# Performance work log

Measured on AMD Instinct MI355X. Metric: run time of the kernel, lower is better.

The kernel has to match this reference:

```python
import jax, jax.numpy as jnp
import numpy as np

D = 1024      # dim_input
H = 16        # n_heads
DH = 64       # dim_inner
S = 1024      # current_seq
M = 1024      # pre_seq (memory)
B = 2         # batch
SCALE = 1.0 / np.sqrt(DH)


def _rel_shift(x):
    # x: [S, J, B, H]; Transformer-XL relative shift
    s, j = x.shape[0], x.shape[1]
    zero = jnp.zeros((s, 1) + x.shape[2:], x.dtype)
    x = jnp.concatenate([zero, x], axis=1)            # [S, J+1, B, H]
    x = x.reshape((j + 1, s) + x.shape[2:])[1:]        # [J, S, B, H]
    return x.reshape((s, j) + x.shape[2:])             # [S, J, B, H]


def setup_inputs() -> dict:
    key = jax.random.key(0)
    ks = jax.random.split(key, 9)
    std = 1.0 / np.sqrt(D)
    return {
        "multi_head_input": jax.random.normal(ks[0], (S, B, D), jnp.float32),
        "position_emb": jax.random.normal(ks[1], (S + M, D), jnp.float32),
        "memory": jax.random.normal(ks[2], (M, B, D), jnp.float32),
        "u": jax.random.normal(ks[3], (H, DH), jnp.float32) * 0.02,
        "v": jax.random.normal(ks[4], (H, DH), jnp.float32) * 0.02,
        "W_kv": jax.random.normal(ks[5], (D, 2 * H * DH), jnp.float32) * std,
        "W_q": jax.random.normal(ks[6], (D, H * DH), jnp.float32) * std,
        "W_pos": jax.random.normal(ks[7], (D, H * DH), jnp.float32) * std,
        "W_out": jax.random.normal(ks[8], (H * DH, D), jnp.float32) * std,
    }


def reference(multi_head_input, position_emb, memory, u, v, W_kv, W_q, W_pos, W_out):
    s = multi_head_input.shape[0]
    m = memory.shape[0]
    b = multi_head_input.shape[1]
    x_mem = jnp.concatenate([memory, multi_head_input], axis=0)   # [M+S, B, D]
    kv = x_mem @ W_kv                                              # [M+S, B, 2*H*DH]
    k, val = jnp.split(kv, 2, axis=-1)
    k = k.reshape(m + s, b, H, DH)
    val = val.reshape(m + s, b, H, DH)
    q = (multi_head_input @ W_q).reshape(s, b, H, DH)              # [S, B, H, DH]

    # content term: (q + u) . k
    content = jnp.einsum('ibhd,jbhd->ijbh', q + u, k)              # [S, M+S, B, H]
    # position term: (q + v) . r, then rel_shift
    r = (position_emb @ W_pos).reshape(m + s, H, DH)               # [M+S, H, DH]
    pos = jnp.einsum('ibhd,jhd->ijbh', q + v, r)                   # [S, M+S, B, H]
    pos = _rel_shift(pos)

    attn = jax.nn.softmax((content + pos) * SCALE, axis=1)         # [S, M+S, B, H]
    out = jnp.einsum('ijbh,jbhd->ibhd', attn, val).reshape(s, b, H * DH)
    return out @ W_out                                             # [S, B, D]
```

## Files before the change

### kernel.cpp

```cpp
#include <hip/hip_runtime.h>
#include <hip/hip_bf16.h>
#include <hip/hip_fp16.h>
#include <math.h>

#define D    1024
#define H    16
#define DH   64
#define S    1024
#define M    1024
#define B    2
#define J    2048
#define SCALE 0.125f

typedef __attribute__((ext_vector_type(8))) short        bf16x8;
typedef __attribute__((ext_vector_type(4))) short        s16x4;
typedef __attribute__((ext_vector_type(8))) _Float16     h16x8;
typedef __attribute__((ext_vector_type(8))) unsigned short us8;
typedef __attribute__((ext_vector_type(4))) float        f32x4;

__device__ __forceinline__ short f2bs(float f) {
    __hip_bfloat16 t = __float2bfloat16(f);
    short r; __builtin_memcpy(&r, &t, 2); return r;
}
__device__ __forceinline__ unsigned short f2bf_fast(float f) {
    unsigned int u; __builtin_memcpy(&u, &f, 4);
    return (unsigned short)((u + 0x8000u) >> 16);
}

__device__ __forceinline__ void g2l16(const short* g, short* l) {
    __builtin_amdgcn_global_load_lds(
        (const __attribute__((address_space(1))) unsigned int*)g,
        (__attribute__((address_space(3))) unsigned int*)l, 16, 0, 0);
}

__global__ __launch_bounds__(256)
void prep(const float* __restrict__ mem, const float* __restrict__ x,
          const float* __restrict__ pemb,
          const float* __restrict__ Wkv, const float* __restrict__ Wq,
          const float* __restrict__ Wpos, const float* __restrict__ Wout,
          short* __restrict__ a_bf, short* __restrict__ p_bf,
          short* __restrict__ wkvt, short* __restrict__ wqt,
          short* __restrict__ wpt,  short* __restrict__ wot)
{
    __shared__ float t[64][65];
    int blk = blockIdx.x;
    const int tid = threadIdx.x;
    if (blk < 6144) {
        const int idx = (blk * 256 + tid) * 4;
        const int TWO_M = 2 * 1024 * 1024;
        float4 v; short* dst;
        if (idx < TWO_M)          { v = *(const float4*)(mem  + idx);           dst = a_bf + idx; }
        else if (idx < 2 * TWO_M) { v = *(const float4*)(x    + idx - TWO_M);   dst = a_bf + idx; }
        else                      { v = *(const float4*)(pemb + idx - 2*TWO_M); dst = p_bf + idx - 2*TWO_M; }
        s16x4 o = { f2bs(v.x), f2bs(v.y), f2bs(v.z), f2bs(v.w) };
        *(s16x4*)dst = o;
        return;
    }
    blk -= 6144;
    const float* src; short* dst; int N, t0;
    if (blk < 512)       { src = Wkv;  dst = wkvt; N = 2048; t0 = blk; }
    else if (blk < 768)  { src = Wq;   dst = wqt;  N = 1024; t0 = blk - 512; }
    else if (blk < 1024) { src = Wpos; dst = wpt;  N = 1024; t0 = blk - 768; }
    else                 { src = Wout; dst = wot;  N = 1024; t0 = blk - 1024; }
    const int ntn = N >> 6;
    const int k0 = (t0 / ntn) * 64, n0 = (t0 % ntn) * 64;
    #pragma unroll
    for (int e = tid; e < 4096; e += 256) {
        int r = e >> 6, c = e & 63;
        t[r][c] = src[(size_t)(k0 + r) * N + n0 + c];
    }
    __syncthreads();
    #pragma unroll
    for (int e = tid; e < 4096; e += 256) {
        int nr = e >> 6, kc = e & 63;
        dst[(size_t)(n0 + nr) * 1024 + k0 + kc] = f2bs(t[kc][nr]);
    }
}

__device__ __forceinline__ void gemm_core(const short* __restrict__ A,
                                          const short* __restrict__ Bt,
                                          short* As, short* Bs,
                                          int bm0, int bn0, int tid,
                                          f32x4 acc[4][4])
{
    const int w    = tid >> 6;
    const int wy   = w >> 1, wx = w & 1;
    const int lane = tid & 63;
    const int lm   = lane & 15;
    const int lq   = lane >> 4;

    for (int k0 = 0; k0 < 1024; k0 += 64) {
        const short* Ab = A  + (size_t)bm0 * 1024 + k0;
        const short* Bb = Bt + (size_t)bn0 * 1024 + k0;
        #pragma unroll
        for (int t = 0; t < 4; ++t) {
            int s = t * 256 + tid;
            int r = s >> 3, c = s & 7;
            int cg = c ^ (r & 7);
            g2l16(Ab + r * 1024 + cg * 8, As + s * 8);
            g2l16(Bb + r * 1024 + cg * 8, Bs + s * 8);
        }
        __syncthreads();
        #pragma unroll
        for (int kk = 0; kk < 2; ++kk) {
            bf16x8 af[4], bg[4];
            #pragma unroll
            for (int r4 = 0; r4 < 4; ++r4) {
                int ar = wy * 64 + r4 * 16 + lm;
                int kc = kk * 4 + lq;
                af[r4] = *(const bf16x8*)(As + ((ar << 3) + (kc ^ (ar & 7))) * 8);
            }
            #pragma unroll
            for (int c4 = 0; c4 < 4; ++c4) {
                int br = wx * 64 + c4 * 16 + lm;
                int kc = kk * 4 + lq;
                bg[c4] = *(const bf16x8*)(Bs + ((br << 3) + (kc ^ (br & 7))) * 8);
            }
            #pragma unroll
            for (int r4 = 0; r4 < 4; ++r4)
                #pragma unroll
                for (int c4 = 0; c4 < 4; ++c4)
                    acc[r4][c4] = __builtin_amdgcn_mfma_f32_16x16x32_bf16(
                        af[r4], bg[c4], acc[r4][c4], 0, 0, 0);
        }
        __syncthreads();
    }
}

__global__ __launch_bounds__(256)
void proj_fused(const short* __restrict__ a_bf, const short* __restrict__ p_bf,
                const short* __restrict__ wkvt, const short* __restrict__ wqt,
                const short* __restrict__ wpt,
                short* __restrict__ k_bf, short* __restrict__ vt_bf,
                short* __restrict__ qu_bf, short* __restrict__ qv_bf,
                short* __restrict__ r_bf,
                const float* __restrict__ uvec, const float* __restrict__ vvec)
{
    __shared__ __align__(16) short As[128 * 64];
    __shared__ __align__(16) short Bs[128 * 64];

    int blk = blockIdx.x;
    int mode, bx, by;
    const short *A, *Bt;
    if (blk < 512)      { bx = blk & 15; by = blk >> 4;
                          if (bx >= 8) { mode = 4; A = wkvt; Bt = a_bf; }
                          else         { mode = 0; A = a_bf; Bt = wkvt; } }
    else if (blk < 640) { int b2 = blk - 512; mode = 1; bx = b2 & 7; by = b2 >> 3;
                          A = a_bf + (size_t)2048 * 1024; Bt = wqt; }
    else                { int b3 = blk - 640; mode = 2; bx = b3 & 7; by = b3 >> 3;
                          A = p_bf; Bt = wpt; }
    const int bn0 = (mode == 4) ? by * 128 : bx * 128;
    const int bm0 = (mode == 4) ? bx * 128 : by * 128;
    const int tid = threadIdx.x;
    const int w = tid >> 6, wy = w >> 1, wx = w & 1;
    const int lane = tid & 63, lm = lane & 15, lq = lane >> 4;

    f32x4 acc[4][4];
    #pragma unroll
    for (int r = 0; r < 4; ++r)
        #pragma unroll
        for (int c = 0; c < 4; ++c) acc[r][c] = (f32x4){0.f, 0.f, 0.f, 0.f};

    gemm_core(A, Bt, As, Bs, bm0, bn0, tid, acc);

    #pragma unroll
    for (int r4 = 0; r4 < 4; ++r4) {
        #pragma unroll
        for (int c4 = 0; c4 < 4; ++c4) {
            const int n = bn0 + wx * 64 + c4 * 16 + lm;
            float ubias = 0.f, vbias = 0.f;
            if (mode == 1) { ubias = uvec[n]; vbias = vvec[n]; }
            #pragma unroll
            for (int reg = 0; reg < 4; ++reg) {
                const int m = bm0 + wy * 64 + r4 * 16 + lq * 4 + reg;
                const float val = acc[r4][c4][reg];
                if (mode == 0) {
                    int j = m >> 1, b = m & 1;
                    int h = n >> 6, d = n & 63;
                    k_bf[(((size_t)b * H + h) * J + j) * DH + d] = f2bs(val);
                } else if (mode == 4) {
                    int n2 = m - 1024, h = n2 >> 6, d = n2 & 63;
                    int j = n >> 1, b = n & 1;
                    vt_bf[(((size_t)b * H + h) * DH + d) * J + j] = f2bs(val);
                } else if (mode == 1) {
                    int i = m >> 1, b = m & 1;
                    int h = n >> 6, d = n & 63;
                    size_t o = (((size_t)b * H + h) * S + i) * DH + d;
                    qu_bf[o] = f2bs((val + ubias) * SCALE);
                    qv_bf[o] = f2bs((val + vbias) * SCALE);
                } else {
                    int h = n >> 6, d = n & 63;
                    r_bf[((size_t)h * J + m) * DH + d] = f2bs(val);
                }
            }
        }
    }
}

__global__ __launch_bounds__(256)
void gemm_out(const short* __restrict__ A, const short* __restrict__ Bt,
              float* __restrict__ out)
{
    __shared__ __align__(16) short As[128 * 64];
    __shared__ __align__(16) short Bs[128 * 64];
    const int bn0 = blockIdx.x * 128, bm0 = blockIdx.y * 128;
    const int tid = threadIdx.x;
    const int w = tid >> 6, wy = w >> 1, wx = w & 1;
    const int lane = tid & 63, lm = lane & 15, lq = lane >> 4;

    f32x4 acc[4][4];
    #pragma unroll
    for (int r = 0; r < 4; ++r)
        #pragma unroll
        for (int c = 0; c < 4; ++c) acc[r][c] = (f32x4){0.f, 0.f, 0.f, 0.f};

    gemm_core(A, Bt, As, Bs, bm0, bn0, tid, acc);

    #pragma unroll
    for (int r4 = 0; r4 < 4; ++r4)
        #pragma unroll
        for (int c4 = 0; c4 < 4; ++c4) {
            const int n = bn0 + wx * 64 + c4 * 16 + lm;
            #pragma unroll
            for (int reg = 0; reg < 4; ++reg) {
                const int m = bm0 + wy * 64 + r4 * 16 + lq * 4 + reg;
                out[(size_t)m * 1024 + n] = acc[r4][c4][reg];
            }
        }
}

__device__ __forceinline__ int sidx(int m, int c) {
    return (m << 10) + (c ^ (m << 3));
}

__global__ __launch_bounds__(512)
void attn_mfma(const short* __restrict__ qu_bf, const short* __restrict__ qv_bf,
               const short* __restrict__ k_bf,  const short* __restrict__ vt_bf,
               const short* __restrict__ r_bf,
               float* __restrict__ opart, float* __restrict__ lsum)
{
    __shared__ __align__(16) unsigned short sc[32 * 1024];
    __half* sch = (__half*)sc;
    float*  scF = (float*)sc;

    const int bh  = blockIdx.x;
    const int it  = blockIdx.y;
    const int jh  = blockIdx.z;
    const int i0  = it * 32;
    const int cbeg = jh << 10, cend = cbeg + 1024;
    const int h   = bh & (H - 1);
    const int tid = threadIdx.x;
    const int w    = tid >> 6;
    const int lane = tid & 63;
    const int lm   = lane & 15;
    const int lq   = lane >> 4;
    const int slot = (it * 32 + bh) * 2 + jh;

    const short* qup0 = qu_bf + ((size_t)(bh * S + i0 + lm)) * DH + lq * 8;
    const short* qup1 = qup0 + 16 * DH;
    bf16x8 au00 = *(const bf16x8*)qup0,        au01 = *(const bf16x8*)(qup0 + 32);
    bf16x8 au10 = *(const bf16x8*)qup1,        au11 = *(const bf16x8*)(qup1 + 32);
    const short* qvp0 = qv_bf + ((size_t)(bh * S + i0 + lm)) * DH + lq * 8;
    const short* qvp1 = qvp0 + 16 * DH;
    bf16x8 av00 = *(const bf16x8*)qvp0,        av01 = *(const bf16x8*)(qvp0 + 32);
    bf16x8 av10 = *(const bf16x8*)qvp1,        av11 = *(const bf16x8*)(qvp1 + 32);
    int r1a = i0 + 1 + lm;  if (r1a > S - 1) r1a = S - 1;
    int r1b = i0 + 17 + lm; if (r1b > S - 1) r1b = S - 1;
    const short* qwp0 = qv_bf + ((size_t)(bh * S + r1a)) * DH + lq * 8;
    const short* qwp1 = qv_bf + ((size_t)(bh * S + r1b)) * DH + lq * 8;
    bf16x8 aw00 = *(const bf16x8*)qwp0,        aw01 = *(const bf16x8*)(qwp0 + 32);
    bf16x8 aw10 = *(const bf16x8*)qwp1,        aw11 = *(const bf16x8*)(qwp1 + 32);

    if (tid < 32) {
        int hole = i0 + tid + 1025;
        if (hole >= cbeg && hole < cend) sc[sidx(tid, hole - cbeg)] = 0;
    }

    const short* rbase = r_bf + (size_t)h * J * DH;

    {
        int tmp = cbeg + 977 - i0;
        int tlo = tmp > 0 ? ((tmp + 15) >> 4) : 0;
        int thi = (cend + 1022 - i0) >> 4; if (thi > 127) thi = 127;
        for (int t = tlo + w; t <= thi; t += 8) {
            const short* rp = rbase + (size_t)(t * 16 + lm) * DH + lq * 8;
            bf16x8 b0 = *(const bf16x8*)rp, b1 = *(const bf16x8*)(rp + 32);
            f32x4 c0 = {0.f,0.f,0.f,0.f}, c1 = {0.f,0.f,0.f,0.f};
            c0 = __builtin_amdgcn_mfma_f32_16x16x32_bf16(av00, b0, c0, 0, 0, 0);
            c1 = __builtin_amdgcn_mfma_f32_16x16x32_bf16(av10, b0, c1, 0, 0, 0);
            c0 = __builtin_amdgcn_mfma_f32_16x16x32_bf16(av01, b1, c0, 0, 0, 0);
            c1 = __builtin_amdgcn_mfma_f32_16x16x32_bf16(av11, b1, c1, 0, 0, 0);
            int cb = i0 + t * 16 + lm - 1023 - cbeg;
            int base = i0 + 16 * t - 1023;
            if (base >= cbeg && base + 46 < cend) {
                #pragma unroll
                for (int r = 0; r < 4; ++r) {
                    int m0 = lq * 4 + r, m1 = m0 + 16;
                    sch[sidx(m0, cb + m0)] = __float2half(c0[r]);
                    sch[sidx(m1, cb + m1)] = __float2half(c1[r]);
                }
            } else {
                #pragma unroll
                for (int r = 0; r < 4; ++r) {
                    int m0 = lq * 4 + r, m1 = m0 + 16;
                    int cA = cb + m0, cB = cb + m1;
                    if (cA >= 0 && cA < 1024) sch[sidx(m0, cA)] = __float2half(c0[r]);
                    if (cB >= 0 && cB < 1024) sch[sidx(m1, cB)] = __float2half(c1[r]);
                }
            }
        }
    }

    {
        int tmpw = cbeg - 1072 - i0;
        int tlw = tmpw > 0 ? ((tmpw + 15) >> 4) : 0;
        int thw = (cend - 1027 - i0) >> 4; if (thw > 127) thw = 127;
        for (int t = tlw + w; t <= thw; t += 8) {
            const short* rp = rbase + (size_t)(t * 16 + lm) * DH + lq * 8;
            bf16x8 b0 = *(const bf16x8*)rp, b1 = *(const bf16x8*)(rp + 32);
            f32x4 c0 = {0.f,0.f,0.f,0.f}, c1 = {0.f,0.f,0.f,0.f};
            c0 = __builtin_amdgcn_mfma_f32_16x16x32_bf16(aw00, b0, c0, 0, 0, 0);
            c1 = __builtin_amdgcn_mfma_f32_16x16x32_bf16(aw10, b0, c1, 0, 0, 0);
            c0 = __builtin_amdgcn_mfma_f32_16x16x32_bf16(aw01, b1, c0, 0, 0, 0);
            c1 = __builtin_amdgcn_mfma_f32_16x16x32_bf16(aw11, b1, c1, 0, 0, 0);
            int cb = i0 + t * 16 + lm + 1026 - cbeg;
            int base = i0 + 16 * t + 1026;
            if (base >= cbeg && base + 46 < cend) {
                #pragma unroll
                for (int r = 0; r < 4; ++r) {
                    int m0 = lq * 4 + r, m1 = m0 + 16;
                    sch[sidx(m0, cb + m0)] = __float2half(c0[r]);
                    sch[sidx(m1, cb + m1)] = __float2half(c1[r]);
                }
            } else {
                #pragma unroll
                for (int r = 0; r < 4; ++r) {
                    int m0 = lq * 4 + r, m1 = m0 + 16;
                    int cA = cb + m0, cB = cb + m1;
                    if (cA >= 0 && cA < 1024) sch[sidx(m0, cA)] = __float2half(c0[r]);
                    if (cB >= 0 && cB < 1024) sch[sidx(m1, cB)] = __float2half(c1[r]);
                }
            }
        }
    }

    const short* kbase = k_bf + (size_t)bh * J * DH;
    int tc0 = jh * 64 + w + 8 * ((it) & 7);
    int tc1 = jh * 64 + w + 8 * ((1 + it) & 7);
    const short* kp0 = kbase + (size_t)(tc0 * 16 + lm) * DH + lq * 8;
    const short* kp1 = kbase + (size_t)(tc1 * 16 + lm) * DH + lq * 8;
    bf16x8 kb0 = *(const bf16x8*)kp0, kb1 = *(const bf16x8*)(kp0 + 32);
    bf16x8 kb2 = *(const bf16x8*)kp1, kb3 = *(const bf16x8*)(kp1 + 32);
    __syncthreads();

    #pragma unroll 1
    for (int g = 0; g < 8; g += 2) {
        int t0 = jh * 64 + w + 8 * ((g + it) & 7);
        int t1 = jh * 64 + w + 8 * ((g + 1 + it) & 7);
        bf16x8 nb0, nb1, nb2, nb3;
        if (g + 2 < 8) {
            int u0 = jh * 64 + w + 8 * ((g + 2 + it) & 7);
            int u1 = jh * 64 + w + 8 * ((g + 3 + it) & 7);
            const short* np0 = kbase + (size_t)(u0 * 16 + lm) * DH + lq * 8;
            const short* np1 = kbase + (size_t)(u1 * 16 + lm) * DH + lq * 8;
            nb0 = *(const bf16x8*)np0; nb1 = *(const bf16x8*)(np0 + 32);
            nb2 = *(const bf16x8*)np1; nb3 = *(const bf16x8*)(np1 + 32);
        }
        int lc0 = t0 * 16 + lm - cbeg;
        int lc1 = t1 * 16 + lm - cbeg;
        f32x4 c0, c1, c2, c3;
        #pragma unroll
        for (int r = 0; r < 4; ++r) {
            c0[r] = __half2float(sch[sidx(lq * 4 + r, lc0)]);
            c1[r] = __half2float(sch[sidx(16 + lq * 4 + r, lc0)]);
            c2[r] = __half2float(sch[sidx(lq * 4 + r, lc1)]);
            c3[r] = __half2float(sch[sidx(16 + lq * 4 + r, lc1)]);
        }
        c0 = __builtin_amdgcn_mfma_f32_16x16x32_bf16(au00, kb0, c0, 0, 0, 0);
        c1 = __builtin_amdgcn_mfma_f32_16x16x32_bf16(au10, kb0, c1, 0, 0, 0);
        c2 = __builtin_amdgcn_mfma_f32_16x16x32_bf16(au00, kb2, c2, 0, 0, 0);
        c3 = __builtin_amdgcn_mfma_f32_16x16x32_bf16(au10, kb2, c3, 0, 0, 0);
        c0 = __builtin_amdgcn_mfma_f32_16x16x32_bf16(au01, kb1, c0, 0, 0, 0);
        c1 = __builtin_amdgcn_mfma_f32_16x16x32_bf16(au11, kb1, c1, 0, 0, 0);
        c2 = __builtin_amdgcn_mfma_f32_16x16x32_bf16(au01, kb3, c2, 0, 0, 0);
        c3 = __builtin_amdgcn_mfma_f32_16x16x32_bf16(au11, kb3, c3, 0, 0, 0);
        #pragma unroll
        for (int r = 0; r < 4; ++r) {
            sch[sidx(lq * 4 + r, lc0)]      = __float2half(c0[r]);
            sch[sidx(16 + lq * 4 + r, lc0)] = __float2half(c1[r]);
            sch[sidx(lq * 4 + r, lc1)]      = __float2half(c2[r]);
            sch[sidx(16 + lq * 4 + r, lc1)] = __float2half(c3[r]);
        }
        kb0 = nb0; kb1 = nb1; kb2 = nb2; kb3 = nb3;
    }
    __syncthreads();

    f32x4 acc[4][2];
    #pragma unroll
    for (int ds = 0; ds < 4; ++ds) {
        acc[ds][0] = (f32x4){0.f, 0.f, 0.f, 0.f};
        acc[ds][1] = (f32x4){0.f, 0.f, 0.f, 0.f};
    }
    float rs0 = 0.f, rs1 = 0.f;
    #pragma unroll 1
    for (int c = 0; c < 4; ++c) {
        int jb = w * 128 + ((c + it) & 3) * 32;
        h16x8 ra0 = *(const h16x8*)(sc + sidx(lm, jb + lq * 8));
        h16x8 ra1 = *(const h16x8*)(sc + sidx(16 + lm, jb + lq * 8));
        bf16x8 bv[4];
        #pragma unroll
        for (int ds = 0; ds < 4; ++ds)
            bv[ds] = *(const bf16x8*)(vt_bf +
                ((size_t)bh * DH + ds * 16 + lm) * J + cbeg + jb + lq * 8);
        us8 pa, pb;
        #pragma unroll
        for (int k = 0; k < 8; ++k) {
            float e0 = __builtin_amdgcn_exp2f((float)ra0[k] * 1.44269504f);
            float e1 = __builtin_amdgcn_exp2f((float)ra1[k] * 1.44269504f);
            rs0 += e0; rs1 += e1;
            pa[k] = f2bf_fast(e0);
            pb[k] = f2bf_fast(e1);
        }
        bf16x8 a0, a1;
        __builtin_memcpy(&a0, &pa, 16);
        __builtin_memcpy(&a1, &pb, 16);
        #pragma unroll
        for (int ds = 0; ds < 4; ++ds) {
            acc[ds][0] = __builtin_amdgcn_mfma_f32_16x16x32_bf16(a0, bv[ds], acc[ds][0], 0, 0, 0);
            acc[ds][1] = __builtin_amdgcn_mfma_f32_16x16x32_bf16(a1, bv[ds], acc[ds][1], 0, 0, 0);
        }
    }
    rs0 += __shfl_xor(rs0, 16); rs0 += __shfl_xor(rs0, 32);
    rs1 += __shfl_xor(rs1, 16); rs1 += __shfl_xor(rs1, 32);
    if (lq == 0) {
        lsum[(size_t)slot * 256 + w * 32 + lm]      = rs0;
        lsum[(size_t)slot * 256 + w * 32 + 16 + lm] = rs1;
    }
    __syncthreads();

    #pragma unroll
    for (int ds = 0; ds < 4; ++ds)
        #pragma unroll
        for (int r = 0; r < 4; ++r) {
            int m0 = lq * 4 + r, m1 = m0 + 16;
            scF[w * 2048 + m0 * 64 + ds * 16 + lm] = acc[ds][0][r];
            scF[w * 2048 + m1 * 64 + ds * 16 + lm] = acc[ds][1][r];
        }
    __syncthreads();

    {
        float* op = opart + (size_t)slot * 2048;
        const int e = tid * 4;
        float4 s = *(const float4*)(scF + e);
        #pragma unroll
        for (int r = 1; r < 8; ++r) {
            float4 t = *(const float4*)(scF + r * 2048 + e);
            s.x += t.x; s.y += t.y; s.z += t.z; s.w += t.w;
        }
        *(float4*)(op + e) = s;
    }
}

__global__ __launch_bounds__(256)
void attn_combine(const float* __restrict__ opart, const float* __restrict__ lsum,
                  short* __restrict__ o_bf)
{
    const int blk = blockIdx.x;
    const int it = blk >> 5, bh = blk & 31;
    const int h = bh & 15, b = bh >> 4;
    __shared__ float wgt[32];
    const int tid = threadIdx.x;
    if (tid < 32) {
        float l = 0.f;
        #pragma unroll
        for (int wv = 0; wv < 8; ++wv)
            l += lsum[(size_t)(blk * 2 + 0) * 256 + wv * 32 + tid]
               + lsum[(size_t)(blk * 2 + 1) * 256 + wv * 32 + tid];
        wgt[tid] = 1.0f / l;
    }
    __syncthreads();
    const float* p0 = opart + (size_t)(blk * 2 + 0) * 2048;
    const float* p1 = opart + (size_t)(blk * 2 + 1) * 2048;
    #pragma unroll
    for (int e = tid; e < 2048; e += 256) {
        int m = e >> 6, d = e & 63;
        float val = (p0[e] + p1[e]) * wgt[m];
        o_bf[((size_t)(it * 32 + m) * B + b) * (H * DH) + h * DH + d] = f2bs(val);
    }
}

extern "C" void kernel_launch(void* const* d_in, const int* in_sizes, int n_in,
                              void* d_out, int out_size, void* d_ws, size_t ws_size,
                              hipStream_t stream)
{
    const float* x    = (const float*)d_in[0];
    const float* pemb = (const float*)d_in[1];
    const float* mem  = (const float*)d_in[2];
    const float* u    = (const float*)d_in[3];
    const float* v    = (const float*)d_in[4];
    const float* Wkv  = (const float*)d_in[5];
    const float* Wq   = (const float*)d_in[6];
    const float* Wpos = (const float*)d_in[7];
    const float* Wout = (const float*)d_in[8];
    float* out = (float*)d_out;

    char* p = (char*)d_ws;
    short* a_bf  = (short*)p; p += (size_t)4096 * 1024 * 2;
    short* p_bf  = (short*)p; p += (size_t)2048 * 1024 * 2;
    short* wkvt  = (short*)p; p += (size_t)2048 * 1024 * 2;
    short* wqt   = (short*)p; p += (size_t)1024 * 1024 * 2;
    short* wpt   = (short*)p; p += (size_t)1024 * 1024 * 2;
    short* wot   = (short*)p; p += (size_t)1024 * 1024 * 2;
    short* k_bf  = (short*)p; p += (size_t)B * H * J * DH * 2;
    short* vt_bf = (short*)p; p += (size_t)B * H * J * DH * 2;
    short* qu_bf = (short*)p; p += (size_t)B * H * S * DH * 2;
    short* qv_bf = (short*)p; p += (size_t)B * H * S * DH * 2;
    short* r_bf  = (short*)p; p += (size_t)H * J * DH * 2;
    short* o_bf  = (short*)p;

    float* opart = (float*)d_ws;
    float* lsum  = (float*)((char*)d_ws + (size_t)16 * 1024 * 1024);

    prep<<<7424, 256, 0, stream>>>(mem, x, pemb, Wkv, Wq, Wpos, Wout,
                                   a_bf, p_bf, wkvt, wqt, wpt, wot);
    proj_fused<<<768, 256, 0, stream>>>(a_bf, p_bf, wkvt, wqt, wpt,
                                        k_bf, vt_bf, qu_bf, qv_bf, r_bf, u, v);
    attn_mfma<<<dim3(B * H, S / 32, 2), 512, 0, stream>>>(
        qu_bf, qv_bf, k_bf, vt_bf, r_bf, opart, lsum);
    attn_combine<<<(S / 32) * B * H, 256, 0, stream>>>(opart, lsum, o_bf);
    gemm_out<<<dim3(8, 16), 256, 0, stream>>>(o_bf, wot, out);
}
```

Before: 295.5 us.

## Split attention key range into four chunks with bf16 partial outputs

Splits the attention key dimension into four 512-wide chunks instead of two, doubling the grid and halving the per-block shared score buffer. The cross-wave reduction now runs in two phases so the halved LDS still fits, and partial outputs are written as bf16 to cut combine traffic. The combine kernel sums four partials. This trades more launched blocks and extra partial/reduction traffic for more parallelism and occupancy, and bf16 partials add some rounding error.

Measured after the change: 321.2 us. 8.7% more time.

```diff
diff --git a/kernel.cpp b/kernel.cpp
--- a/kernel.cpp
+++ b/kernel.cpp
@@ -21,6 +21,10 @@
 __device__ __forceinline__ short f2bs(float f) {
     __hip_bfloat16 t = __float2bfloat16(f);
     short r; __builtin_memcpy(&r, &t, 2); return r;
+}
+__device__ __forceinline__ float bs2f(short s) {
+    unsigned int u = ((unsigned int)(unsigned short)s) << 16;
+    float f; __builtin_memcpy(&f, &u, 4); return f;
 }
 __device__ __forceinline__ unsigned short f2bf_fast(float f) {
     unsigned int u; __builtin_memcpy(&u, &f, 4);
@@ -230,31 +234,31 @@
 }
 
 __device__ __forceinline__ int sidx(int m, int c) {
-    return (m << 10) + (c ^ (m << 3));
+    return (m << 9) + (c ^ (m << 3));
 }
 
 __global__ __launch_bounds__(512)
 void attn_mfma(const short* __restrict__ qu_bf, const short* __restrict__ qv_bf,
                const short* __restrict__ k_bf,  const short* __restrict__ vt_bf,
                const short* __restrict__ r_bf,
-               float* __restrict__ opart, float* __restrict__ lsum)
-{
-    __shared__ __align__(16) unsigned short sc[32 * 1024];
+               short* __restrict__ opart, float* __restrict__ lsum)
+{
+    __shared__ __align__(16) unsigned short sc[32 * 512];
     __half* sch = (__half*)sc;
     float*  scF = (float*)sc;
 
     const int bh  = blockIdx.x;
     const int it  = blockIdx.y;
-    const int jh  = blockIdx.z;
+    const int jq  = blockIdx.z;
     const int i0  = it * 32;
-    const int cbeg = jh << 10, cend = cbeg + 1024;
+    const int cbeg = jq << 9, cend = cbeg + 512;
     const int h   = bh & (H - 1);
     const int tid = threadIdx.x;
     const int w    = tid >> 6;
     const int lane = tid & 63;
     const int lm   = lane & 15;
     const int lq   = lane >> 4;
-    const int slot = (it * 32 + bh) * 2 + jh;
+    const int slot = (it * 32 + bh) * 4 + jq;
 
     const short* qup0 = qu_bf + ((size_t)(bh * S + i0 + lm)) * DH + lq * 8;
     const short* qup1 = qup0 + 16 * DH;
@@ -304,8 +308,8 @@
                 for (int r = 0; r < 4; ++r) {
                     int m0 = lq * 4 + r, m1 = m0 + 16;
                     int cA = cb + m0, cB = cb + m1;
-                    if (cA >= 0 && cA < 1024) sch[sidx(m0, cA)] = __float2half(c0[r]);
-                    if (cB >= 0 && cB < 1024) sch[sidx(m1, cB)] = __float2half(c1[r]);
+                    if (cA >= 0 && cA < 512) sch[sidx(m0, cA)] = __float2half(c0[r]);
+                    if (cB >= 0 && cB < 512) sch[sidx(m1, cB)] = __float2half(c1[r]);
                 }
             }
         }
@@ -337,16 +341,17 @@
                 for (int r = 0; r < 4; ++r) {
                     int m0 = lq * 4 + r, m1 = m0 + 16;
                     int cA = cb + m0, cB = cb + m1;
-                    if (cA >= 0 && cA < 1024) sch[sidx(m0, cA)] = __float2half(c0[r]);
-                    if (cB >= 0 && cB < 1024) sch[sidx(m1, cB)] = __float2half(c1[r]);
+                    if (cA >= 0 && cA < 512) sch[sidx(m0, cA)] = __float2half(c0[r]);
+                    if (cB >= 0 && cB < 512) sch[sidx(m1, cB)] = __float2half(c1[r]);
                 }
             }
         }
     }
 
     const short* kbase = k_bf + (size_t)bh * J * DH;
-    int tc0 = jh * 64 + w + 8 * ((it) & 7);
-    int tc1 = jh * 64 + w + 8 * ((1 + it) & 7);
+    const int tb0 = cbeg >> 4;
+    int tc0 = tb0 + w + 8 * ((it) & 3);
+    int tc1 = tb0 + w + 8 * ((1 + it) & 3);
     const short* kp0 = kbase + (size_t)(tc0 * 16 + lm) * DH + lq * 8;
     const short* kp1 = kbase + (size_t)(tc1 * 16 + lm) * DH + lq * 8;
     bf16x8 kb0 = *(const bf16x8*)kp0, kb1 = *(const bf16x8*)(kp0 + 32);
@@ -354,13 +359,13 @@
     __syncthreads();
 
     #pragma unroll 1
-    for (int g = 0; g < 8; g += 2) {
-        int t0 = jh * 64 + w + 8 * ((g + it) & 7);
-        int t1 = jh * 64 + w + 8 * ((g + 1 + it) & 7);
+    for (int g = 0; g < 4; g += 2) {
+        int t0 = tb0 + w + 8 * ((g + it) & 3);
+        int t1 = tb0 + w + 8 * ((g + 1 + it) & 3);
         bf16x8 nb0, nb1, nb2, nb3;
-        if (g + 2 < 8) {
-            int u0 = jh * 64 + w + 8 * ((g + 2 + it) & 7);
-            int u1 = jh * 64 + w + 8 * ((g + 3 + it) & 7);
+        if (g + 2 < 4) {
+            int u0 = tb0 + w + 8 * ((g + 2 + it) & 3);
+            int u1 = tb0 + w + 8 * ((g + 3 + it) & 3);
             const short* np0 = kbase + (size_t)(u0 * 16 + lm) * DH + lq * 8;
             const short* np1 = kbase + (size_t)(u1 * 16 + lm) * DH + lq * 8;
             nb0 = *(const bf16x8*)np0; nb1 = *(const bf16x8*)(np0 + 32);
@@ -403,8 +408,8 @@
     }
     float rs0 = 0.f, rs1 = 0.f;
     #pragma unroll 1
-    for (int c = 0; c < 4; ++c) {
-        int jb = w * 128 + ((c + it) & 3) * 32;
+    for (int c = 0; c < 2; ++c) {
+        int jb = w * 64 + ((c + it) & 1) * 32;
         h16x8 ra0 = *(const h16x8*)(sc + sidx(lm, jb + lq * 8));
         h16x8 ra1 = *(const h16x8*)(sc + sidx(16 + lm, jb + lq * 8));
         bf16x8 bv[4];
@@ -438,31 +443,45 @@
     }
     __syncthreads();
 
-    #pragma unroll
-    for (int ds = 0; ds < 4; ++ds)
-        #pragma unroll
-        for (int r = 0; r < 4; ++r) {
-            int m0 = lq * 4 + r, m1 = m0 + 16;
-            scF[w * 2048 + m0 * 64 + ds * 16 + lm] = acc[ds][0][r];
-            scF[w * 2048 + m1 * 64 + ds * 16 + lm] = acc[ds][1][r];
-        }
+    if (w < 4) {
+        #pragma unroll
+        for (int ds = 0; ds < 4; ++ds)
+            #pragma unroll
+            for (int r = 0; r < 4; ++r) {
+                int m0 = lq * 4 + r, m1 = m0 + 16;
+                scF[w * 2048 + m0 * 64 + ds * 16 + lm] = acc[ds][0][r];
+                scF[w * 2048 + m1 * 64 + ds * 16 + lm] = acc[ds][1][r];
+            }
+    }
+    __syncthreads();
+    if (w >= 4) {
+        #pragma unroll
+        for (int ds = 0; ds < 4; ++ds)
+            #pragma unroll
+            for (int r = 0; r < 4; ++r) {
+                int m0 = lq * 4 + r, m1 = m0 + 16;
+                scF[(w - 4) * 2048 + m0 * 64 + ds * 16 + lm] += acc[ds][0][r];
+                scF[(w - 4) * 2048 + m1 * 64 + ds * 16 + lm] += acc[ds][1][r];
+            }
+    }
     __syncthreads();
 
     {
-        float* op = opart + (size_t)slot * 2048;
+        short* op = opart + (size_t)slot * 2048;
         const int e = tid * 4;
         float4 s = *(const float4*)(scF + e);
         #pragma unroll
-        for (int r = 1; r < 8; ++r) {
+        for (int r = 1; r < 4; ++r) {
             float4 t = *(const float4*)(scF + r * 2048 + e);
             s.x += t.x; s.y += t.y; s.z += t.z; s.w += t.w;
         }
-        *(float4*)(op + e) = s;
+        s16x4 o = { f2bs(s.x), f2bs(s.y), f2bs(s.z), f2bs(s.w) };
+        *(s16x4*)(op + e) = o;
     }
 }
 
 __global__ __launch_bounds__(256)
-void attn_combine(const float* __restrict__ opart, const float* __restrict__ lsum,
+void attn_combine(const short* __restrict__ opart, const float* __restrict__ lsum,
                   short* __restrict__ o_bf)
 {
     const int blk = blockIdx.x;
@@ -473,19 +492,22 @@
     if (tid < 32) {
         float l = 0.f;
         #pragma unroll
-        for (int wv = 0; wv < 8; ++wv)
-            l += lsum[(size_t)(blk * 2 + 0) * 256 + wv * 32 + tid]
-               + lsum[(size_t)(blk * 2 + 1) * 256 + wv * 32 + tid];
+        for (int q = 0; q < 4; ++q)
+            #pragma unroll
+            for (int wv = 0; wv < 8; ++wv)
+                l += lsum[(size_t)(blk * 4 + q) * 256 + wv * 32 + tid];
         wgt[tid] = 1.0f / l;
     }
     __syncthreads();
-    const float* p0 = opart + (size_t)(blk * 2 + 0) * 2048;
-    const float* p1 = opart + (size_t)(blk * 2 + 1) * 2048;
     #pragma unroll
     for (int e = tid; e < 2048; e += 256) {
+        float val = bs2f(opart[(size_t)(blk * 4 + 0) * 2048 + e])
+                  + bs2f(opart[(size_t)(blk * 4 + 1) * 2048 + e])
+                  + bs2f(opart[(size_t)(blk * 4 + 2) * 2048 + e])
+                  + bs2f(opart[(size_t)(blk * 4 + 3) * 2048 + e]);
         int m = e >> 6, d = e & 63;
-        float val = (p0[e] + p1[e]) * wgt[m];
-        o_bf[((size_t)(it * 32 + m) * B + b) * (H * DH) + h * DH + d] = f2bs(val);
+        o_bf[((size_t)(it * 32 + m) * B + b) * (H * DH) + h * DH + d] =
+            f2bs(val * wgt[m]);
     }
 }
 
@@ -518,14 +540,14 @@
     short* r_bf  = (short*)p; p += (size_t)H * J * DH * 2;
     short* o_bf  = (short*)p;
 
-    float* opart = (float*)d_ws;
+    short* opart = (short*)d_ws;
     float* lsum  = (float*)((char*)d_ws + (size_t)16 * 1024 * 1024);
 
     prep<<<7424, 256, 0, stream>>>(mem, x, pemb, Wkv, Wq, Wpos, Wout,
                                    a_bf, p_bf, wkvt, wqt, wpt, wot);
     proj_fused<<<768, 256, 0, stream>>>(a_bf, p_bf, wkvt, wqt, wpt,
                                         k_bf, vt_bf, qu_bf, qv_bf, r_bf, u, v);
-    attn_mfma<<<dim3(B * H, S / 32, 2), 512, 0, stream>>>(
+    attn_mfma<<<dim3(B * H, S / 32, 4), 512, 0, stream>>>(
         qu_bf, qv_bf, k_bf, vt_bf, r_bf, opart, lsum);
     attn_combine<<<(S / 32) * B * H, 256, 0, stream>>>(opart, lsum, o_bf);
     gemm_out<<<dim3(8, 16), 256, 0, stream>>>(o_bf, wot, out);
```
